# Performance work log

Hardware: AMD Instinct MI355X
Metric: run time of the kernel (lower is better)

The kernel has to match this reference:

```python
import jax, jax.numpy as jnp
import numpy as np

B, T, F_IN = 8, 32768, 64
N, F, HID = 64, 64, 32


def setup_inputs() -> dict:
    key = jax.random.key(0)
    ks = jax.random.split(key, 10)
    x = jax.random.normal(ks[0], (B, T, F_IN), dtype=jnp.float32)
    # pre_mlp: Dense(32) -> relu -> Dense(F)
    W1 = jax.random.normal(ks[1], (F_IN, HID), dtype=jnp.float32) * (1.0 / np.sqrt(F_IN))
    b1 = jnp.zeros((HID,), dtype=jnp.float32)
    W2 = jax.random.normal(ks[2], (HID, F), dtype=jnp.float32) * (1.0 / np.sqrt(HID))
    b2 = jnp.zeros((F,), dtype=jnp.float32)
    # SSM params (inits mirror the flax module)
    Lambda_raw = -0.7 * jnp.ones((N,), dtype=jnp.float32)
    P = jax.random.normal(ks[3], (N,), dtype=jnp.float32) * 0.02
    Wu = jax.random.normal(ks[4], (F,), dtype=jnp.float32) * 0.02
    C = jax.random.normal(ks[5], (N,), dtype=jnp.float32) * 0.02
    D = jax.random.normal(ks[6], (F,), dtype=jnp.float32) * 0.02
    b_y = jnp.zeros((), dtype=jnp.float32)
    return {"x": x, "W1": W1, "b1": b1, "W2": W2, "b2": b2,
            "Lambda_raw": Lambda_raw, "P": P, "Wu": Wu, "C": C, "D": D, "b_y": b_y}


def reference(x, W1, b1, W2, b2, Lambda_raw, P, Wu, C, D, b_y):
    # pre_mlp: per-timestep feature projection
    h = jax.nn.relu(jnp.einsum('bti,ih->bth', x, W1) + b1)
    feats = jnp.einsum('bth,hf->btf', h, W2) + b2          # (B,T,F)
    # scalar drive per timestep
    u = jnp.einsum('btf,f->bt', feats, Wu)                 # (B,T)
    # stable diagonal decay in (0,1): Lambda = -softplus(raw), A = exp(Lambda)
    A = jnp.exp(-jax.nn.softplus(Lambda_raw))              # (N,)
    Bu = u[..., None] * P                                  # (B,T,N) per-step injection

    def step(s, bu_t):                                     # s: (B,N), bu_t: (B,N)
        s = A * s + bu_t
        return s, s

    s0 = jnp.zeros((x.shape[0], Lambda_raw.shape[0]), dtype=x.dtype)
    _, states = jax.lax.scan(step, s0, jnp.swapaxes(Bu, 0, 1))  # (T,B,N)
    states = jnp.swapaxes(states, 0, 1)                    # (B,T,N)
    # readout: C-state + D-feedthrough + bias
    y = jnp.einsum('btn,n->bt', states, C) + jnp.einsum('btf,f->bt', feats, D) + b_y
    return y
```

## Files before the change

kernel.cpp:

```cpp
#include <hip/hip_runtime.h>
#include <hip/hip_bf16.h>

#define BB   8
#define TT   32768
#define FIN  64
#define HIDN 32
#define NST  64
#define FFD  64
#define WWIN 256
#define TILE 1024
#define TPW  4

typedef __attribute__((ext_vector_type(8))) short short8;
typedef __attribute__((ext_vector_type(4))) float f32x4;

static __device__ __forceinline__ unsigned short f2bf(float f) {
    unsigned int u = __builtin_bit_cast(unsigned int, f);
    unsigned int lsb = (u >> 16) & 1u;
    u += 0x7fffu + lsb;
    return (unsigned short)(u >> 16);
}

static __device__ __forceinline__ float dot8(float4 a0, float4 a1, float4 b0, float4 b1) {
    return a0.x*b0.x + a0.y*b0.y + a0.z*b0.z + a0.w*b0.w
         + a1.x*b1.x + a1.y*b1.y + a1.z*b1.z + a1.w*b1.w;
}

static __device__ __forceinline__ short8 pack_bf8(float4 a, float4 b) {
    union { short8 s8; __hip_bfloat162 b2[4]; } u;
    u.b2[0] = __float22bfloat162_rn({a.x, a.y});
    u.b2[1] = __float22bfloat162_rn({a.z, a.w});
    u.b2[2] = __float22bfloat162_rn({b.x, b.y});
    u.b2[3] = __float22bfloat162_rn({b.z, b.w});
    return u.s8;
}

__global__ __launch_bounds__(256) void mlp_kernel(
    const float* __restrict__ x, const float* __restrict__ W1,
    const float* __restrict__ b1, const float* __restrict__ W2,
    const float* __restrict__ b2, const float* __restrict__ Wu,
    const float* __restrict__ Dv, const float* __restrict__ b_y,
    float* __restrict__ u, float* __restrict__ yd)
{
    __shared__ __align__(16) uint4 fragLDS[4 * 64];
    __shared__ float pu[32 * 8], pd[32 * 8], pc[16];
    __shared__ __align__(16) float wuF[32], wdF[32];
    __shared__ float cucd[2];

    int tid = threadIdx.x;

    {
        int f    = tid >> 6;
        int lane = tid & 63;
        int khalf = f & 1, ntile = f >> 1;
        int quad  = lane >> 4;
        int nn    = (lane & 15) + ntile * 16;
        unsigned short h8[8];
#pragma unroll
        for (int j = 0; j < 8; ++j) {
            int k = khalf * 32 + quad * 8 + j;
            h8[j] = f2bf(W1[k * HIDN + nn]);
        }
        fragLDS[tid] = make_uint4(
            (unsigned int)h8[0] | ((unsigned int)h8[1] << 16),
            (unsigned int)h8[2] | ((unsigned int)h8[3] << 16),
            (unsigned int)h8[4] | ((unsigned int)h8[5] << 16),
            (unsigned int)h8[6] | ((unsigned int)h8[7] << 16));
    }
    {
        int h = tid >> 3, part = tid & 7;
        const float4* w2p = (const float4*)(W2 + h * FFD + part * 8);
        float4 wa = w2p[0], wb = w2p[1];
        float4 ua = *(const float4*)(Wu + part * 8);
        float4 ub = *(const float4*)(Wu + part * 8 + 4);
        float4 da = *(const float4*)(Dv + part * 8);
        float4 db = *(const float4*)(Dv + part * 8 + 4);
        pu[tid] = dot8(wa, wb, ua, ub);
        pd[tid] = dot8(wa, wb, da, db);
        if (tid < 8) {
            float4 ba = *(const float4*)(b2 + tid * 8);
            float4 bb = *(const float4*)(b2 + tid * 8 + 4);
            float4 u2a = *(const float4*)(Wu + tid * 8);
            float4 u2b = *(const float4*)(Wu + tid * 8 + 4);
            pc[tid] = dot8(ba, bb, u2a, u2b);
        } else if (tid < 16) {
            int p = tid - 8;
            float4 ba = *(const float4*)(b2 + p * 8);
            float4 bb = *(const float4*)(b2 + p * 8 + 4);
            float4 d2a = *(const float4*)(Dv + p * 8);
            float4 d2b = *(const float4*)(Dv + p * 8 + 4);
            pc[tid] = dot8(ba, bb, d2a, d2b);
        }
    }
    __syncthreads();
    if (tid < 32) {
        float s = 0.f;
#pragma unroll
        for (int p = 0; p < 8; ++p) s += pu[tid * 8 + p];
        wuF[tid] = s;
    } else if (tid < 64) {
        int h = tid - 32;
        float s = 0.f;
#pragma unroll
        for (int p = 0; p < 8; ++p) s += pd[h * 8 + p];
        wdF[h] = s;
    } else if (tid == 64) {
        float s = 0.f;
#pragma unroll
        for (int p = 0; p < 8; ++p) s += pc[p];
        cucd[0] = s;
    } else if (tid == 65) {
        float s = 0.f;
#pragma unroll
        for (int p = 8; p < 16; ++p) s += pc[p];
        cucd[1] = s + b_y[0];
    }
    __syncthreads();

    int lane = tid & 63, wid = tid >> 6;
    int m = lane & 15, quad = lane >> 4;

    short8 bk0n0 = __builtin_bit_cast(short8, fragLDS[0 * 64 + lane]);
    short8 bk1n0 = __builtin_bit_cast(short8, fragLDS[1 * 64 + lane]);
    short8 bk0n1 = __builtin_bit_cast(short8, fragLDS[2 * 64 + lane]);
    short8 bk1n1 = __builtin_bit_cast(short8, fragLDS[3 * 64 + lane]);

    float4 b1A = *(const float4*)&b1[quad * 4];
    float4 b1B = *(const float4*)&b1[16 + quad * 4];
    float4 wuA = *(const float4*)&wuF[quad * 4];
    float4 wuB = *(const float4*)&wuF[16 + quad * 4];
    float4 wdA = *(const float4*)&wdF[quad * 4];
    float4 wdB = *(const float4*)&wdF[16 + quad * 4];
    float cu = cucd[0], cd = cucd[1];

    int tbase = blockIdx.x * 256 + wid * 64;
    const float* xr = x + (size_t)(tbase + m) * FIN + quad * 8;

    float4 xv[2][4];
#define LOADT(buf, tt) { const float* p_ = xr + (tt) * 16 * FIN;          \
        (buf)[0] = *(const float4*)(p_);      (buf)[1] = *(const float4*)(p_ + 4);  \
        (buf)[2] = *(const float4*)(p_ + 32); (buf)[3] = *(const float4*)(p_ + 36); }

    LOADT(xv[0], 0);
    LOADT(xv[1], 1);

#pragma unroll
    for (int tt = 0; tt < TPW; ++tt) {
        float4 x0 = xv[tt & 1][0], x1 = xv[tt & 1][1];
        float4 x2 = xv[tt & 1][2], x3 = xv[tt & 1][3];
        if (tt + 2 < TPW) LOADT(xv[tt & 1], tt + 2);

        short8 a0 = pack_bf8(x0, x1);
        short8 a1 = pack_bf8(x2, x3);

        f32x4 acc0 = {0.f, 0.f, 0.f, 0.f};
        f32x4 acc1 = {0.f, 0.f, 0.f, 0.f};
        acc0 = __builtin_amdgcn_mfma_f32_16x16x32_bf16(bk0n0, a0, acc0, 0, 0, 0);
        acc0 = __builtin_amdgcn_mfma_f32_16x16x32_bf16(bk1n0, a1, acc0, 0, 0, 0);
        acc1 = __builtin_amdgcn_mfma_f32_16x16x32_bf16(bk0n1, a0, acc1, 0, 0, 0);
        acc1 = __builtin_amdgcn_mfma_f32_16x16x32_bf16(bk1n1, a1, acc1, 0, 0, 0);

        float ut = 0.f, yt = 0.f, h;
        h = fmaxf(acc0[0] + b1A.x, 0.f); ut += h * wuA.x; yt += h * wdA.x;
        h = fmaxf(acc0[1] + b1A.y, 0.f); ut += h * wuA.y; yt += h * wdA.y;
        h = fmaxf(acc0[2] + b1A.z, 0.f); ut += h * wuA.z; yt += h * wdA.z;
        h = fmaxf(acc0[3] + b1A.w, 0.f); ut += h * wuA.w; yt += h * wdA.w;
        h = fmaxf(acc1[0] + b1B.x, 0.f); ut += h * wuB.x; yt += h * wdB.x;
        h = fmaxf(acc1[1] + b1B.y, 0.f); ut += h * wuB.y; yt += h * wdB.y;
        h = fmaxf(acc1[2] + b1B.z, 0.f); ut += h * wuB.z; yt += h * wdB.z;
        h = fmaxf(acc1[3] + b1B.w, 0.f); ut += h * wuB.w; yt += h * wdB.w;

        ut += __shfl_xor(ut, 16); ut += __shfl_xor(ut, 32);
        yt += __shfl_xor(yt, 16); yt += __shfl_xor(yt, 32);

        if (lane < 16) {
            int row = tbase + tt * 16 + lane;
            u[row]  = ut + cu;
            yd[row] = yt + cd;
        }
    }
#undef LOADT
}

__global__ __launch_bounds__(256) void conv_kernel(
    const float* __restrict__ u, const float* __restrict__ Lraw,
    const float* __restrict__ P, const float* __restrict__ C,
    float* __restrict__ y)
{
    __shared__ __align__(16) float us[WWIN + TILE];
    __shared__ __align__(16) float Ks[WWIN];
    __shared__ float spv[NST], cpv[NST];

    int tid = threadIdx.x;
    const int blocksPerSeq = TT / TILE;
    int b  = blockIdx.x / blocksPerSeq;
    int t0 = (blockIdx.x % blocksPerSeq) * TILE;
    const float* ub = u + (size_t)b * TT;

    for (int s = tid; s < WWIN + TILE; s += 256) {
        int gt = t0 - WWIN + s;
        us[s] = (gt >= 0) ? ub[gt] : 0.f;
    }
    if (tid < NST) {
        float raw = Lraw[tid];
        spv[tid] = fmaxf(raw, 0.f) + log1pf(expf(-fabsf(raw)));
        cpv[tid] = C[tid] * P[tid];
    }
    __syncthreads();
    {
        float jf = (float)tid;
        float acc = 0.f;
#pragma unroll 4
        for (int n = 0; n < NST; ++n) acc += cpv[n] * __expf(-spv[n] * jf);
        Ks[tid] = acc;
    }
    __syncthreads();

    int base = WWIN + tid * 4;
    size_t oidx = (size_t)b * TT + t0 + tid * 4;
    float4 yv = *(const float4*)&y[oidx];
    float a0 = yv.x, a1 = yv.y, a2 = yv.z, a3 = yv.w;

#pragma unroll 8
    for (int j = 0; j < WWIN; j += 4) {
        float4 kk = *(const float4*)&Ks[j];
        float4 ua = *(const float4*)&us[base - j - 4];
        float4 ux = *(const float4*)&us[base - j];
        a0 += kk.x * ux.x + kk.y * ua.w + kk.z * ua.z + kk.w * ua.y;
        a1 += kk.x * ux.y + kk.y * ux.x + kk.z * ua.w + kk.w * ua.z;
        a2 += kk.x * ux.z + kk.y * ux.y + kk.z * ux.x + kk.w * ua.w;
        a3 += kk.x * ux.w + kk.y * ux.z + kk.z * ux.y + kk.w * ux.x;
    }
    *(float4*)&y[oidx] = make_float4(a0, a1, a2, a3);
}

extern "C" void kernel_launch(void* const* d_in, const int* in_sizes, int n_in,
                              void* d_out, int out_size, void* d_ws, size_t ws_size,
                              hipStream_t stream)
{
    const float* x    = (const float*)d_in[0];
    const float* W1   = (const float*)d_in[1];
    const float* b1   = (const float*)d_in[2];
    const float* W2   = (const float*)d_in[3];
    const float* b2   = (const float*)d_in[4];
    const float* Lraw = (const float*)d_in[5];
    const float* P    = (const float*)d_in[6];
    const float* Wu   = (const float*)d_in[7];
    const float* C    = (const float*)d_in[8];
    const float* Dv   = (const float*)d_in[9];
    const float* b_y  = (const float*)d_in[10];

    float* u = (float*)d_ws;
    float* y = (float*)d_out;

    mlp_kernel<<<(BB * TT) / 256, 256, 0, stream>>>(x, W1, b1, W2, b2, Wu, Dv, b_y, u, y);
    conv_kernel<<<(BB * TT) / TILE, 256, 0, stream>>>(u, Lraw, P, C, y);
}
```

Measured before the change: 123.5 us.

## Fuse MLP and convolution kernels into one tile kernel with halo recompute

Merges the MLP projection and causal-convolution kernels into a single kernel that keeps the drive signal and feedthrough in shared memory, recomputing the MLP for a 256-step halo per tile. This removes the global round-trip of u and y and one kernel launch. In exchange each block reads about 25% extra x rows, and the grid shrinks to 256 blocks of 512 threads, which may reduce latency hiding. The convolution is split across two thread halves whose partial sums are combined through shared memory.

```diff
diff --git a/kernel.cpp b/kernel.cpp
--- a/kernel.cpp
+++ b/kernel.cpp
@@ -9,7 +9,10 @@
 #define FFD  64
 #define WWIN 256
 #define TILE 1024
-#define TPW  4
+#define NTHR 512
+#define ROWS (WWIN + TILE)
+#define RPW  (ROWS / 8)
+#define TPW  (RPW / 16)
 
 typedef __attribute__((ext_vector_type(8))) short short8;
 typedef __attribute__((ext_vector_type(4))) float f32x4;
@@ -35,30 +38,38 @@
     return u.s8;
 }
 
-__global__ __launch_bounds__(256) void mlp_kernel(
+__global__ __launch_bounds__(NTHR) void fused_kernel(
     const float* __restrict__ x, const float* __restrict__ W1,
     const float* __restrict__ b1, const float* __restrict__ W2,
-    const float* __restrict__ b2, const float* __restrict__ Wu,
-    const float* __restrict__ Dv, const float* __restrict__ b_y,
-    float* __restrict__ u, float* __restrict__ yd)
+    const float* __restrict__ b2, const float* __restrict__ Lraw,
+    const float* __restrict__ P, const float* __restrict__ Wu,
+    const float* __restrict__ C, const float* __restrict__ Dv,
+    const float* __restrict__ b_y, float* __restrict__ y)
 {
     __shared__ __align__(16) uint4 fragLDS[4 * 64];
     __shared__ float pu[32 * 8], pd[32 * 8], pc[16];
     __shared__ __align__(16) float wuF[32], wdF[32];
     __shared__ float cucd[2];
+    __shared__ float spv[NST], cpv[NST];
+    __shared__ __align__(16) float us[ROWS];
+    __shared__ __align__(16) float yv[TILE];
+    __shared__ __align__(16) float Ks[WWIN];
+    __shared__ __align__(16) float ypart[TILE];
 
     int tid = threadIdx.x;
-
-    {
-        int f    = tid >> 6;
-        int lane = tid & 63;
+    int b   = blockIdx.x >> 5;
+    int t0  = (blockIdx.x & 31) * TILE;
+
+    if (tid < 256) {
+        int f     = tid >> 6;
+        int lane_ = tid & 63;
         int khalf = f & 1, ntile = f >> 1;
-        int quad  = lane >> 4;
-        int nn    = (lane & 15) + ntile * 16;
+        int qd    = lane_ >> 4;
+        int nn    = (lane_ & 15) + ntile * 16;
         unsigned short h8[8];
 #pragma unroll
         for (int j = 0; j < 8; ++j) {
-            int k = khalf * 32 + quad * 8 + j;
+            int k = khalf * 32 + qd * 8 + j;
             h8[j] = f2bf(W1[k * HIDN + nn]);
         }
         fragLDS[tid] = make_uint4(
@@ -66,8 +77,7 @@
             (unsigned int)h8[2] | ((unsigned int)h8[3] << 16),
             (unsigned int)h8[4] | ((unsigned int)h8[5] << 16),
             (unsigned int)h8[6] | ((unsigned int)h8[7] << 16));
-    }
-    {
+
         int h = tid >> 3, part = tid & 7;
         const float4* w2p = (const float4*)(W2 + h * FFD + part * 8);
         float4 wa = w2p[0], wb = w2p[1];
@@ -92,7 +102,13 @@
             pc[tid] = dot8(ba, bb, d2a, d2b);
         }
     }
+    if (tid < NST) {
+        float raw = Lraw[tid];
+        spv[tid] = fmaxf(raw, 0.f) + log1pf(expf(-fabsf(raw)));
+        cpv[tid] = C[tid] * P[tid];
+    }
     __syncthreads();
+
     if (tid < 32) {
         float s = 0.f;
 #pragma unroll
@@ -114,6 +130,13 @@
 #pragma unroll
         for (int p = 8; p < 16; ++p) s += pc[p];
         cucd[1] = s + b_y[0];
+    }
+    if (tid < WWIN) {
+        float jf = (float)tid;
+        float acc = 0.f;
+#pragma unroll 4
+        for (int n = 0; n < NST; ++n) acc += cpv[n] * __expf(-spv[n] * jf);
+        Ks[tid] = acc;
     }
     __syncthreads();
 
@@ -133,12 +156,14 @@
     float4 wdB = *(const float4*)&wdF[16 + quad * 4];
     float cu = cucd[0], cd = cucd[1];
 
-    int tbase = blockIdx.x * 256 + wid * 64;
-    const float* xr = x + (size_t)(tbase + m) * FIN + quad * 8;
+    int wstart = wid * RPW;
+    int gbase  = t0 - WWIN + wstart;
+    const float* xb = x + (size_t)b * TT * FIN + quad * 8;
 
     float4 xv[2][4];
-#define LOADT(buf, tt) { const float* p_ = xr + (tt) * 16 * FIN;          \
-        (buf)[0] = *(const float4*)(p_);      (buf)[1] = *(const float4*)(p_ + 4);  \
+#define LOADT(buf, tt) { int g_ = gbase + (tt) * 16 + m; if (g_ < 0) g_ = 0;      \
+        const float* p_ = xb + (size_t)g_ * FIN;                                   \
+        (buf)[0] = *(const float4*)(p_);      (buf)[1] = *(const float4*)(p_ + 4); \
         (buf)[2] = *(const float4*)(p_ + 32); (buf)[3] = *(const float4*)(p_ + 36); }
 
     LOADT(xv[0], 0);
@@ -174,64 +199,46 @@
         yt += __shfl_xor(yt, 16); yt += __shfl_xor(yt, 32);
 
         if (lane < 16) {
-            int row = tbase + tt * 16 + lane;
-            u[row]  = ut + cu;
-            yd[row] = yt + cd;
+            int local = wstart + tt * 16 + lane;
+            int g = gbase + tt * 16 + lane;
+            us[local] = (g >= 0) ? (ut + cu) : 0.f;
+            if (local >= WWIN) yv[local - WWIN] = yt + cd;
         }
     }
 #undef LOADT
-}
-
-__global__ __launch_bounds__(256) void conv_kernel(
-    const float* __restrict__ u, const float* __restrict__ Lraw,
-    const float* __restrict__ P, const float* __restrict__ C,
-    float* __restrict__ y)
-{
-    __shared__ __align__(16) float us[WWIN + TILE];
-    __shared__ __align__(16) float Ks[WWIN];
-    __shared__ float spv[NST], cpv[NST];
-
-    int tid = threadIdx.x;
-    const int blocksPerSeq = TT / TILE;
-    int b  = blockIdx.x / blocksPerSeq;
-    int t0 = (blockIdx.x % blocksPerSeq) * TILE;
-    const float* ub = u + (size_t)b * TT;
-
-    for (int s = tid; s < WWIN + TILE; s += 256) {
-        int gt = t0 - WWIN + s;
-        us[s] = (gt >= 0) ? ub[gt] : 0.f;
-    }
-    if (tid < NST) {
-        float raw = Lraw[tid];
-        spv[tid] = fmaxf(raw, 0.f) + log1pf(expf(-fabsf(raw)));
-        cpv[tid] = C[tid] * P[tid];
-    }
     __syncthreads();
+
     {
-        float jf = (float)tid;
-        float acc = 0.f;
-#pragma unroll 4
-        for (int n = 0; n < NST; ++n) acc += cpv[n] * __expf(-spv[n] * jf);
-        Ks[tid] = acc;
-    }
-    __syncthreads();
-
-    int base = WWIN + tid * 4;
-    size_t oidx = (size_t)b * TT + t0 + tid * 4;
-    float4 yv = *(const float4*)&y[oidx];
-    float a0 = yv.x, a1 = yv.y, a2 = yv.z, a3 = yv.w;
-
+        int half = tid >> 8;
+        int q    = tid & 255;
+        int o    = q * 4;
+        int base = WWIN + o;
+        float a0, a1, a2, a3;
+        if (half == 0) {
+            float4 y4 = *(const float4*)&yv[o];
+            a0 = y4.x; a1 = y4.y; a2 = y4.z; a3 = y4.w;
+        } else {
+            a0 = a1 = a2 = a3 = 0.f;
+        }
+        int j0 = half * 128;
 #pragma unroll 8
-    for (int j = 0; j < WWIN; j += 4) {
-        float4 kk = *(const float4*)&Ks[j];
-        float4 ua = *(const float4*)&us[base - j - 4];
-        float4 ux = *(const float4*)&us[base - j];
-        a0 += kk.x * ux.x + kk.y * ua.w + kk.z * ua.z + kk.w * ua.y;
-        a1 += kk.x * ux.y + kk.y * ux.x + kk.z * ua.w + kk.w * ua.z;
-        a2 += kk.x * ux.z + kk.y * ux.y + kk.z * ux.x + kk.w * ua.w;
-        a3 += kk.x * ux.w + kk.y * ux.z + kk.z * ux.y + kk.w * ux.x;
-    }
-    *(float4*)&y[oidx] = make_float4(a0, a1, a2, a3);
+        for (int j = j0; j < j0 + 128; j += 4) {
+            float4 kk = *(const float4*)&Ks[j];
+            float4 ua = *(const float4*)&us[base - j - 4];
+            float4 ux = *(const float4*)&us[base - j];
+            a0 += kk.x * ux.x + kk.y * ua.w + kk.z * ua.z + kk.w * ua.y;
+            a1 += kk.x * ux.y + kk.y * ux.x + kk.z * ua.w + kk.w * ua.z;
+            a2 += kk.x * ux.z + kk.y * ux.y + kk.z * ux.x + kk.w * ua.w;
+            a3 += kk.x * ux.w + kk.y * ux.z + kk.z * ux.y + kk.w * ux.x;
+        }
+        if (half == 1) *(float4*)&ypart[o] = make_float4(a0, a1, a2, a3);
+        __syncthreads();
+        if (half == 0) {
+            float4 p4 = *(const float4*)&ypart[o];
+            size_t oidx = (size_t)b * TT + t0 + o;
+            *(float4*)&y[oidx] = make_float4(a0 + p4.x, a1 + p4.y, a2 + p4.z, a3 + p4.w);
+        }
+    }
 }
 
 extern "C" void kernel_launch(void* const* d_in, const int* in_sizes, int n_in,
@@ -250,9 +257,9 @@
     const float* Dv   = (const float*)d_in[9];
     const float* b_y  = (const float*)d_in[10];
 
-    float* u = (float*)d_ws;
     float* y = (float*)d_out;
-
-    mlp_kernel<<<(BB * TT) / 256, 256, 0, stream>>>(x, W1, b1, W2, b2, Wu, Dv, b_y, u, y);
-    conv_kernel<<<(BB * TT) / TILE, 256, 0, stream>>>(u, Lraw, P, C, y);
-}
+    (void)d_ws; (void)ws_size;
+
+    fused_kernel<<<(BB * TT) / TILE, NTHR, 0, stream>>>(
+        x, W1, b1, W2, b2, Lraw, P, Wu, C, Dv, b_y, y);
+}
```

Measured after the change: 123.1 us. About the same (-0.3%).
